# Kernel optimization log

Hardware: AMD Instinct MI355X
Metric: run time of the kernel (lower is better)

Reference implementation:

```python
import jax, jax.numpy as jnp
import numpy as np
from functools import partial

VOCAB = 32000
EMB = 512
HID = 1024
DEPTH = 2
B, S = 4, 512
PAD = 0


def _lstm_layer(x, mask, Wk, Wr, b):
    """Keras-style LSTM (gates i,f,g,o), return_sequences, zero init state.
    x: [B,S,D], mask: [B,S] bool. Masked steps carry state & output through."""
    Bdim = x.shape[0]
    units = Wr.shape[0]
    h0 = jnp.zeros((Bdim, units), x.dtype)
    c0 = jnp.zeros((Bdim, units), x.dtype)

    def step(carry, inp):
        h, c = carry
        xt, mt = inp                      # xt [B,D], mt [B]
        z = xt @ Wk + h @ Wr + b          # [B,4U]
        i, f, g, o = jnp.split(z, 4, axis=-1)
        i = jax.nn.sigmoid(i)
        f = jax.nn.sigmoid(f)
        g = jnp.tanh(g)
        o = jax.nn.sigmoid(o)
        c_new = f * c + i * g
        h_new = o * jnp.tanh(c_new)
        m = mt[:, None]
        h = jnp.where(m, h_new, h)
        c = jnp.where(m, c_new, c)
        return (h, c), h

    xs = jnp.swapaxes(x, 0, 1)            # [S,B,D]
    ms = jnp.swapaxes(mask, 0, 1)         # [S,B]
    _, ys = jax.lax.scan(step, (h0, c0), (xs, ms))
    return jnp.swapaxes(ys, 0, 1)         # [B,S,U]


def setup_inputs() -> dict:
    key = jax.random.key(0)
    ks = jax.random.split(key, 10)
    r = 0.02  # initializer_range
    inputs = jax.random.randint(ks[0], (B, S), 0, VOCAB, dtype=jnp.int32)
    emb = jax.random.normal(ks[1], (VOCAB, EMB), jnp.float32) * r
    Wk0 = jax.random.normal(ks[2], (EMB, 4 * HID), jnp.float32) * r
    Wr0 = jax.random.normal(ks[3], (HID, 4 * HID), jnp.float32) * r
    b0 = jnp.zeros((4 * HID,), jnp.float32)
    Wk1 = jax.random.normal(ks[4], (HID, 4 * HID), jnp.float32) * r
    Wr1 = jax.random.normal(ks[5], (HID, 4 * HID), jnp.float32) * r
    b1 = jnp.zeros((4 * HID,), jnp.float32)
    Wp = jax.random.normal(ks[6], (HID, EMB), jnp.float32) * r
    bp = jnp.zeros((EMB,), jnp.float32)
    return {"inputs": inputs, "emb": emb, "Wk0": Wk0, "Wr0": Wr0, "b0": b0,
            "Wk1": Wk1, "Wr1": Wr1, "b1": b1, "Wp": Wp, "bp": bp}


def reference(inputs, emb, Wk0, Wr0, b0, Wk1, Wr1, b1, Wp, bp):
    mask = inputs != PAD                          # [B,S] bool
    fmask = mask.astype(jnp.float32)[..., None]   # [B,S,1]
    x = emb[inputs]                               # [B,S,EMB] embedding lookup
    x = _lstm_layer(x, mask, Wk0, Wr0, b0)        # [B,S,HID]
    x = _lstm_layer(x, mask, Wk1, Wr1, b1)        # [B,S,HID]
    x = x @ Wp + bp                               # [B,S,EMB] output projection
    logits = jnp.einsum('bse,ve->bsv', x, emb)    # tied softmax weights
    onehot0 = jnp.zeros((VOCAB,), jnp.float32).at[0].set(1.0)  # eye(V)[0]
    logits = logits * fmask + onehot0 * (1.0 - fmask)
    return logits
```

## Files before the change

kernel.cpp:

```cpp
#include <hip/hip_runtime.h>

#define VOCAB 32000
#define EMBD  512
#define HIDD  1024
#define SLEN  512
#define NBAT  4
#define GATE4 4096
#define ABLK  128
#define BBLK  128

typedef unsigned long long u64;

#define AL(p) __hip_atomic_load((p), __ATOMIC_RELAXED, __HIP_MEMORY_SCOPE_AGENT)
#define AS(p, v) __hip_atomic_store((p), (v), __ATOMIC_RELAXED, __HIP_MEMORY_SCOPE_AGENT)

__device__ __forceinline__ float2 u2f(u64 x) {
  return make_float2(__uint_as_float((unsigned)x),
                     __uint_as_float((unsigned)(x >> 32)));
}

__global__ __launch_bounds__(256) void transpose_k(const float* __restrict__ src,
                                                   float* __restrict__ dst) {
  __shared__ float t[32][33];
  const int bx = blockIdx.x * 32;
  const int by = blockIdx.y * 32;
  const int r0 = threadIdx.x >> 5;
  const int c  = threadIdx.x & 31;
  #pragma unroll
  for (int i = 0; i < 4; i++) {
    const int r = r0 + i*8;
    t[r][c] = src[(size_t)(by + r)*GATE4 + bx + c];
  }
  __syncthreads();
  #pragma unroll
  for (int i = 0; i < 4; i++) {
    const int rw = r0 + i*8;
    dst[(size_t)(bx + rw)*HIDD + by + c] = t[c][rw];
  }
}

__global__ __launch_bounds__(256) void gemm_nn_emb(
    const int* __restrict__ ids, const float* __restrict__ emb,
    const float* __restrict__ B, const float* __restrict__ bias,
    float* __restrict__ C, int N, int K) {
  __shared__ float As[16][64];
  __shared__ float Bs[16][64];
  const int tid = threadIdx.x;
  const int bm = blockIdx.y * 64;
  const int bn = blockIdx.x * 64;
  const int tx = tid & 15, ty = tid >> 4;
  const int mA = tid >> 2, kqA = (tid & 3) * 4;
  const int kB = tid >> 4, nB = (tid & 15) * 4;
  const int rid = ids[bm + mA];
  float acc[4][4] = {{0.f}};
  for (int k0 = 0; k0 < K; k0 += 16) {
    float4 a4 = *(const float4*)(emb + (size_t)rid*EMBD + k0 + kqA);
    As[kqA+0][mA] = a4.x; As[kqA+1][mA] = a4.y;
    As[kqA+2][mA] = a4.z; As[kqA+3][mA] = a4.w;
    *(float4*)&Bs[kB][nB] = *(const float4*)(B + (size_t)(k0 + kB)*N + bn + nB);
    __syncthreads();
    #pragma unroll
    for (int k = 0; k < 16; k++) {
      float4 av = *(float4*)&As[k][ty*4];
      float4 bv = *(float4*)&Bs[k][tx*4];
      float ar[4] = {av.x, av.y, av.z, av.w};
      float br[4] = {bv.x, bv.y, bv.z, bv.w};
      #pragma unroll
      for (int i = 0; i < 4; i++)
        #pragma unroll
        for (int j = 0; j < 4; j++)
          acc[i][j] += ar[i] * br[j];
    }
    __syncthreads();
  }
  float4 bi = *(const float4*)(bias + bn + tx*4);
  #pragma unroll
  for (int i = 0; i < 4; i++) {
    float4 o;
    o.x = acc[i][0] + bi.x; o.y = acc[i][1] + bi.y;
    o.z = acc[i][2] + bi.z; o.w = acc[i][3] + bi.w;
    *(float4*)(C + (size_t)(bm + ty*4 + i)*N + bn + tx*4) = o;
  }
}

__global__ __launch_bounds__(256) void gemm_nn_bias(
    const float* __restrict__ A, const float* __restrict__ B,
    const float* __restrict__ bias, float* __restrict__ C,
    int M, int N, int K) {
  __shared__ float As[16][64];
  __shared__ float Bs[16][64];
  const int tid = threadIdx.x;
  const int bm = blockIdx.y * 64;
  const int bn = blockIdx.x * 64;
  const int tx = tid & 15, ty = tid >> 4;
  const int mA = tid >> 2, kqA = (tid & 3) * 4;
  const int kB = tid >> 4, nB = (tid & 15) * 4;
  float acc[4][4] = {{0.f}};
  for (int k0 = 0; k0 < K; k0 += 16) {
    float4 a4 = *(const float4*)(A + (size_t)(bm + mA)*K + k0 + kqA);
    As[kqA+0][mA] = a4.x; As[kqA+1][mA] = a4.y;
    As[kqA+2][mA] = a4.z; As[kqA+3][mA] = a4.w;
    *(float4*)&Bs[kB][nB] = *(const float4*)(B + (size_t)(k0 + kB)*N + bn + nB);
    __syncthreads();
    #pragma unroll
    for (int k = 0; k < 16; k++) {
      float4 av = *(float4*)&As[k][ty*4];
      float4 bv = *(float4*)&Bs[k][tx*4];
      float ar[4] = {av.x, av.y, av.z, av.w};
      float br[4] = {bv.x, bv.y, bv.z, bv.w};
      #pragma unroll
      for (int i = 0; i < 4; i++)
        #pragma unroll
        for (int j = 0; j < 4; j++)
          acc[i][j] += ar[i] * br[j];
    }
    __syncthreads();
  }
  float4 bi = *(const float4*)(bias + bn + tx*4);
  #pragma unroll
  for (int i = 0; i < 4; i++) {
    float4 o;
    o.x = acc[i][0] + bi.x; o.y = acc[i][1] + bi.y;
    o.z = acc[i][2] + bi.z; o.w = acc[i][3] + bi.w;
    *(float4*)(C + (size_t)(bm + ty*4 + i)*N + bn + tx*4) = o;
  }
}

__global__ __launch_bounds__(256) void gemm_nt_logits128(
    const float* __restrict__ A,
    const float* __restrict__ Bt,
    const int* __restrict__ ids,
    float* __restrict__ C) {
  const int K = EMBD, N = VOCAB;
  __shared__ float As[16][128];
  __shared__ float Bs[16][128];
  const int tid = threadIdx.x;
  const int bm = blockIdx.y * 128;
  const int bn = blockIdx.x * 128;
  const int tx = tid & 15, ty = tid >> 4;
  const int rL = tid >> 1, kL = (tid & 1) * 8;
  float acc[8][8] = {{0.f}};
  for (int k0 = 0; k0 < K; k0 += 16) {
    float4 a0 = *(const float4*)(A  + (size_t)(bm + rL)*K + k0 + kL);
    float4 a1 = *(const float4*)(A  + (size_t)(bm + rL)*K + k0 + kL + 4);
    float4 b0 = *(const float4*)(Bt + (size_t)(bn + rL)*K + k0 + kL);
    float4 b1 = *(const float4*)(Bt + (size_t)(bn + rL)*K + k0 + kL + 4);
    __syncthreads();
    As[kL+0][rL] = a0.x; As[kL+1][rL] = a0.y; As[kL+2][rL] = a0.z; As[kL+3][rL] = a0.w;
    As[kL+4][rL] = a1.x; As[kL+5][rL] = a1.y; As[kL+6][rL] = a1.z; As[kL+7][rL] = a1.w;
    Bs[kL+0][rL] = b0.x; Bs[kL+1][rL] = b0.y; Bs[kL+2][rL] = b0.z; Bs[kL+3][rL] = b0.w;
    Bs[kL+4][rL] = b1.x; Bs[kL+5][rL] = b1.y; Bs[kL+6][rL] = b1.z; Bs[kL+7][rL] = b1.w;
    __syncthreads();
    #pragma unroll
    for (int k = 0; k < 16; k++) {
      float4 av0 = *(float4*)&As[k][ty*4];
      float4 av1 = *(float4*)&As[k][64 + ty*4];
      float4 bv0 = *(float4*)&Bs[k][tx*4];
      float4 bv1 = *(float4*)&Bs[k][64 + tx*4];
      float ar[8] = {av0.x, av0.y, av0.z, av0.w, av1.x, av1.y, av1.z, av1.w};
      float br[8] = {bv0.x, bv0.y, bv0.z, bv0.w, bv1.x, bv1.y, bv1.z, bv1.w};
      #pragma unroll
      for (int i = 0; i < 8; i++)
        #pragma unroll
        for (int j = 0; j < 8; j++)
          acc[i][j] += ar[i] * br[j];
    }
  }
  #pragma unroll
  for (int i = 0; i < 8; i++) {
    const int row = bm + ((i < 4) ? (ty*4 + i) : (64 + ty*4 + i - 4));
    const bool mk = ids[row] != 0;
    float4 o0, o1;
    if (mk) {
      o0 = make_float4(acc[i][0], acc[i][1], acc[i][2], acc[i][3]);
      o1 = make_float4(acc[i][4], acc[i][5], acc[i][6], acc[i][7]);
    } else {
      o0 = make_float4((bn + tx*4 == 0) ? 1.f : 0.f, 0.f, 0.f, 0.f);
      o1 = make_float4(0.f, 0.f, 0.f, 0.f);
    }
    *(float4*)(C + (size_t)row*N + bn + tx*4)      = o0;
    *(float4*)(C + (size_t)row*N + bn + 64 + tx*4) = o1;
  }
}

__device__ __forceinline__ int rev5(int l) {
  return ((l & 1) << 4) | ((l & 2) << 2) | (l & 4) | ((l & 8) >> 2) | ((l & 16) >> 4);
}

#define HALVE(MASK, SH, HSZ)                          \
    { const int bit_ = (lane >> SH) & 1;              \
      _Pragma("unroll")                               \
      for (int j = 0; j < HSZ; j++) {                 \
        float snd = bit_ ? a[j] : a[j + HSZ];         \
        float kep = bit_ ? a[j + HSZ] : a[j];         \
        a[j] = kep + __shfl_xor(snd, MASK);           \
      } }

__global__ __launch_bounds__(256, 1) void lstm_fused(
    const float* __restrict__ Z0,
    const float* __restrict__ Wr0T,
    const float* __restrict__ Wk1T,
    const float* __restrict__ Wr1T,
    const float* __restrict__ bias1,
    const int* __restrict__ ids,
    float* __restrict__ H1,
    float* __restrict__ H0full,
    unsigned* __restrict__ flgA,
    unsigned* __restrict__ flgB) {
  __shared__ float wk[32][1024];
  __shared__ float z_s[4][64];
  __shared__ float zc[128];
  const int tid  = threadIdx.x;
  const int lane = tid & 63;
  const int w    = tid >> 6;
  const int ccH  = tid >> 7;
  const int part = tid & 127;

  if (blockIdx.x < ABLK) {
    const int hbase = blockIdx.x * 8;
    float4 Wf[16], Wg[16];
    #pragma unroll
    for (int cl = 0; cl < 16; cl++) {
      const int cc = ccH * 16 + cl;
      const int g  = cc >> 3, d = cc & 7;
      const size_t col = (size_t)(g * HIDD + hbase + d);
      Wf[cl] = *(const float4*)(Wr0T + col * HIDD + 4 * part);
      Wg[cl] = *(const float4*)(Wr0T + col * HIDD + 512 + 4 * part);
    }
    float c_reg = 0.f, h_reg = 0.f;
    __syncthreads();

    for (int t = 0; t < SLEN; t++) {
      float pz0 = 0.f, pz1 = 0.f, pz2 = 0.f, pz3 = 0.f;
      int pmk = 0;
      if (tid < 32) {
        const int b = tid >> 3, d = tid & 7;
        const float* zrow = Z0 + (size_t)(b*SLEN + t) * GATE4 + hbase + d;
        pz0 = zrow[0];      pz1 = zrow[HIDD];
        pz2 = zrow[2*HIDD]; pz3 = zrow[3*HIDD];
        pmk = ids[b*SLEN + t];
      }
      float4 ha[NBAT], hb[NBAT];
      if (t > 0) {
        if (tid < ABLK) {
          while (AL(flgA + tid * 16) < (unsigned)t)
            __builtin_amdgcn_s_sleep(1);
        }
        __syncthreads();
        const u64* src = (const u64*)H0full + (size_t)(t - 1) * 2048;
        u64 v[16];
        #pragma unroll
        for (int b = 0; b < NBAT; b++) {
          v[b*4+0] = AL(src + b*512 + 2*part);
          v[b*4+1] = AL(src + b*512 + 2*part + 1);
          v[b*4+2] = AL(src + b*512 + 256 + 2*part);
          v[b*4+3] = AL(src + b*512 + 256 + 2*part + 1);
        }
        #pragma unroll
        for (int b = 0; b < NBAT; b++) {
          float2 p0 = u2f(v[b*4+0]), p1 = u2f(v[b*4+1]);
          float2 q0 = u2f(v[b*4+2]), q1 = u2f(v[b*4+3]);
          ha[b] = make_float4(p0.x, p0.y, p1.x, p1.y);
          hb[b] = make_float4(q0.x, q0.y, q1.x, q1.y);
        }
      } else {
        #pragma unroll
        for (int b = 0; b < NBAT; b++) {
          ha[b] = make_float4(0.f, 0.f, 0.f, 0.f);
          hb[b] = make_float4(0.f, 0.f, 0.f, 0.f);
        }
      }
      float a[64];
      #pragma unroll
      for (int cl = 0; cl < 16; cl++)
        #pragma unroll
        for (int b = 0; b < NBAT; b++)
          a[cl*4 + b] = Wf[cl].x*ha[b].x + Wf[cl].y*ha[b].y
                      + Wf[cl].z*ha[b].z + Wf[cl].w*ha[b].w
                      + Wg[cl].x*hb[b].x + Wg[cl].y*hb[b].y
                      + Wg[cl].z*hb[b].z + Wg[cl].w*hb[b].w;
      #pragma unroll
      for (int i = 0; i < 64; i++) a[i] += __shfl_xor(a[i], 32);
      HALVE(1, 0, 32) HALVE(2, 1, 16) HALVE(4, 2, 8) HALVE(8, 3, 4) HALVE(16, 4, 2)
      if (lane < 32) {
        z_s[w][rev5(lane)*2 + 0] = a[0];
        z_s[w][rev5(lane)*2 + 1] = a[1];
      }
      __syncthreads();
      if (tid < 128) {
        const int cc = tid >> 2, b = tid & 3;
        const int cH = cc >> 4, i = ((cc & 15) << 2) | b;
        zc[tid] = z_s[2*cH][i] + z_s[2*cH + 1][i];
      }
      __syncthreads();
      if (tid < 32) {
        const int b = tid >> 3, d = tid & 7;
        const float zi = zc[((0*8 + d) << 2) + b] + pz0;
        const float zf = zc[((1*8 + d) << 2) + b] + pz1;
        const float zg = zc[((2*8 + d) << 2) + b] + pz2;
        const float zo = zc[((3*8 + d) << 2) + b] + pz3;
        const float ig = 1.f / (1.f + expf(-zi));
        const float fg = 1.f / (1.f + expf(-zf));
        const float gg = tanhf(zg);
        const float og = 1.f / (1.f + expf(-zo));
        const float cn = fg * c_reg + ig * gg;
        const float hn = og * tanhf(cn);
        const bool mk = pmk != 0;
        const float ho = mk ? hn : h_reg;
        c_reg = mk ? cn : c_reg;
        h_reg = ho;
        AS(H0full + (size_t)t * (NBAT*HIDD) + b*HIDD + hbase + d, ho);
      }
      if (w == 0) {
        asm volatile("s_waitcnt vmcnt(0)" ::: "memory");
        if (tid == 0)
          AS(flgA + blockIdx.x * 16, (unsigned)(t + 1));
      }
      __syncthreads();
    }
  } else {
    const int bid = blockIdx.x - ABLK;
    const int ub  = bid * 8;
    for (int i = tid; i < 32 * 256; i += 256) {
      const int c2 = i >> 8, k4 = i & 255;
      const size_t col = (size_t)((c2 >> 3) * HIDD + ub + (c2 & 7));
      *(float4*)&wk[c2][k4 * 4] = *(const float4*)(Wk1T + col * HIDD + 4 * k4);
    }
    float4 Rf[16], Rg[16];
    #pragma unroll
    for (int cl = 0; cl < 16; cl++) {
      const int cc = ccH * 16 + cl;
      const int g  = cc >> 3, d = cc & 7;
      const size_t col = (size_t)(g * HIDD + ub + d);
      Rf[cl] = *(const float4*)(Wr1T + col * HIDD + 4 * part);
      Rg[cl] = *(const float4*)(Wr1T + col * HIDD + 512 + 4 * part);
    }
    float pbi = 0.f, pbf = 0.f, pbg = 0.f, pbo = 0.f;
    if (tid < 32) {
      const int d = tid & 7;
      pbi = bias1[0*HIDD + ub + d];
      pbf = bias1[1*HIDD + ub + d];
      pbg = bias1[2*HIDD + ub + d];
      pbo = bias1[3*HIDD + ub + d];
    }
    float c_reg = 0.f, h_reg = 0.f;
    __syncthreads();

    for (int t = 0; t < SLEN; t++) {
      int pmk = 0;
      if (tid < 32) pmk = ids[(tid >> 3) * SLEN + t];
      if (tid < 128) {
        while (AL(flgA + tid * 16) < (unsigned)(t + 1))
          __builtin_amdgcn_s_sleep(1);
      } else {
        while (AL(flgB + (tid - 128) * 16) < (unsigned)t)
          __builtin_amdgcn_s_sleep(1);
      }
      __syncthreads();
      const u64* h0p = (const u64*)H0full + (size_t)t * 2048;
      u64 v0[16];
      #pragma unroll
      for (int b = 0; b < NBAT; b++) {
        v0[b*4+0] = AL(h0p + b*512 + 2*part);
        v0[b*4+1] = AL(h0p + b*512 + 2*part + 1);
        v0[b*4+2] = AL(h0p + b*512 + 256 + 2*part);
        v0[b*4+3] = AL(h0p + b*512 + 256 + 2*part + 1);
      }
      u64 v1[16];
      if (t > 0) {
        const u64* h1p = (const u64*)H1;
        #pragma unroll
        for (int b = 0; b < NBAT; b++) {
          const size_t row = (size_t)(b*SLEN + t - 1) * 512;
          v1[b*4+0] = AL(h1p + row + 2*part);
          v1[b*4+1] = AL(h1p + row + 2*part + 1);
          v1[b*4+2] = AL(h1p + row + 256 + 2*part);
          v1[b*4+3] = AL(h1p + row + 256 + 2*part + 1);
        }
      } else {
        #pragma unroll
        for (int r = 0; r < 16; r++) v1[r] = 0ull;
      }
      float a[64];
      #pragma unroll
      for (int cl = 0; cl < 16; cl++) {
        const int c2 = ccH * 16 + cl;
        const float4 kf = *(const float4*)&wk[c2][4 * part];
        const float4 kg = *(const float4*)&wk[c2][512 + 4 * part];
        #pragma unroll
        for (int b = 0; b < NBAT; b++) {
          const float2 p0 = u2f(v0[b*4+0]), p1 = u2f(v0[b*4+1]);
          const float2 q0 = u2f(v0[b*4+2]), q1 = u2f(v0[b*4+3]);
          a[cl*4 + b] = kf.x*p0.x + kf.y*p0.y + kf.z*p1.x + kf.w*p1.y
                      + kg.x*q0.x + kg.y*q0.y + kg.z*q1.x + kg.w*q1.y;
        }
      }
      #pragma unroll
      for (int cl = 0; cl < 16; cl++) {
        #pragma unroll
        for (int b = 0; b < NBAT; b++) {
          const float2 p0 = u2f(v1[b*4+0]), p1 = u2f(v1[b*4+1]);
          const float2 q0 = u2f(v1[b*4+2]), q1 = u2f(v1[b*4+3]);
          a[cl*4 + b] += Rf[cl].x*p0.x + Rf[cl].y*p0.y + Rf[cl].z*p1.x + Rf[cl].w*p1.y
                       + Rg[cl].x*q0.x + Rg[cl].y*q0.y + Rg[cl].z*q1.x + Rg[cl].w*q1.y;
        }
      }
      #pragma unroll
      for (int i = 0; i < 64; i++) a[i] += __shfl_xor(a[i], 32);
      HALVE(1, 0, 32) HALVE(2, 1, 16) HALVE(4, 2, 8) HALVE(8, 3, 4) HALVE(16, 4, 2)
      if (lane < 32) {
        z_s[w][rev5(lane)*2 + 0] = a[0];
        z_s[w][rev5(lane)*2 + 1] = a[1];
      }
      __syncthreads();
      if (tid < 128) {
        const int cc = tid >> 2, b = tid & 3;
        const int cH = cc >> 4, i = ((cc & 15) << 2) | b;
        zc[tid] = z_s[2*cH][i] + z_s[2*cH + 1][i];
      }
      __syncthreads();
      if (tid < 32) {
        const int b = tid >> 3, d = tid & 7;
        const float zi = zc[((0*8 + d) << 2) + b] + pbi;
        const float zf = zc[((1*8 + d) << 2) + b] + pbf;
        const float zg = zc[((2*8 + d) << 2) + b] + pbg;
        const float zo = zc[((3*8 + d) << 2) + b] + pbo;
        const float ig = 1.f / (1.f + expf(-zi));
        const float fg = 1.f / (1.f + expf(-zf));
        const float gg = tanhf(zg);
        const float og = 1.f / (1.f + expf(-zo));
        const float cn = fg * c_reg + ig * gg;
        const float hn = og * tanhf(cn);
        const bool mk = pmk != 0;
        const float ho = mk ? hn : h_reg;
        c_reg = mk ? cn : c_reg;
        h_reg = ho;
        AS(H1 + (size_t)(b*SLEN + t) * HIDD + ub + d, ho);
      }
      if (w == 0) {
        asm volatile("s_waitcnt vmcnt(0)" ::: "memory");
        if (tid == 0)
          AS(flgB + bid * 16, (unsigned)(t + 1));
      }
      __syncthreads();
    }
  }
}
#undef HALVE

extern "C" void kernel_launch(void* const* d_in, const int* in_sizes, int n_in,
                              void* d_out, int out_size, void* d_ws, size_t ws_size,
                              hipStream_t stream) {
  const int*   ids = (const int*)  d_in[0];
  const float* emb = (const float*)d_in[1];
  const float* Wk0 = (const float*)d_in[2];
  const float* Wr0 = (const float*)d_in[3];
  const float* b0  = (const float*)d_in[4];
  const float* Wk1 = (const float*)d_in[5];
  const float* Wr1 = (const float*)d_in[6];
  const float* b1  = (const float*)d_in[7];
  const float* Wp  = (const float*)d_in[8];
  const float* bp  = (const float*)d_in[9];
  float* out = (float*)d_out;

  float* Z      = out;
  float* H1     = out + 8388608;
  float* Wr0T   = out + 10485760;
  float* Wr1T   = out + 14680064;
  float* Wk1T   = out + 18874368;
  float* H0full = out + 23068672;
  unsigned* flgA = (unsigned*)d_ws;
  unsigned* flgB = (unsigned*)d_ws + 2048;
  float* P   = ((float*)d_ws) + 4096;

  hipMemsetAsync(d_ws, 0, 16384, stream);
  transpose_k<<<dim3(128, 32), 256, 0, stream>>>(Wr0, Wr0T);
  transpose_k<<<dim3(128, 32), 256, 0, stream>>>(Wr1, Wr1T);
  transpose_k<<<dim3(128, 32), 256, 0, stream>>>(Wk1, Wk1T);
  gemm_nn_emb<<<dim3(64, 32), 256, 0, stream>>>(ids, emb, Wk0, b0, Z, 4096, 512);
  lstm_fused<<<ABLK + BBLK, 256, 0, stream>>>(Z, Wr0T, Wk1T, Wr1T, b1, ids,
                                              H1, H0full, flgA, flgB);
  gemm_nn_bias<<<dim3(8, 32), 256, 0, stream>>>(H1, Wp, bp, P, 2048, 512, 1024);
  gemm_nt_logits128<<<dim3(250, 16), 256, 0, stream>>>(P, emb, ids, out);
}
```

Measured before the change: 4.819 ms.

## Stage hidden state through LDS with coalesced loads; split layer-1 wait for overlap

Hidden-state vectors (H0 and H1) are now loaded cooperatively by all 256 threads with contiguous 64-bit atomic loads, staged in a 16KB shared buffer, and read back as float4 per thread. Before, each thread issued strided per-batch atomic loads and many threads read the same data. In layer 1, the wait on layer-1 flags (flgB) is moved after the input-projection matmul on h0, so the h0 contribution is computed while the recurrent dependency resolves. The cost is extra __syncthreads barriers and more LDS use on top of a block that already holds 128KB of weights in LDS.

```diff
diff --git a/kernel.cpp b/kernel.cpp
--- a/kernel.cpp
+++ b/kernel.cpp
@@ -13,11 +13,6 @@
 
 #define AL(p) __hip_atomic_load((p), __ATOMIC_RELAXED, __HIP_MEMORY_SCOPE_AGENT)
 #define AS(p, v) __hip_atomic_store((p), (v), __ATOMIC_RELAXED, __HIP_MEMORY_SCOPE_AGENT)
-
-__device__ __forceinline__ float2 u2f(u64 x) {
-  return make_float2(__uint_as_float((unsigned)x),
-                     __uint_as_float((unsigned)(x >> 32)));
-}
 
 __global__ __launch_bounds__(256) void transpose_k(const float* __restrict__ src,
                                                    float* __restrict__ dst) {
@@ -208,6 +203,7 @@
     unsigned* __restrict__ flgA,
     unsigned* __restrict__ flgB) {
   __shared__ float wk[32][1024];
+  __shared__ float hs[NBAT * HIDD];
   __shared__ float z_s[4][64];
   __shared__ float zc[128];
   const int tid  = threadIdx.x;
@@ -248,20 +244,18 @@
         }
         __syncthreads();
         const u64* src = (const u64*)H0full + (size_t)(t - 1) * 2048;
-        u64 v[16];
+        u64 v[8];
+        #pragma unroll
+        for (int r = 0; r < 8; r++)
+          v[r] = AL(src + tid + (r << 8));
+        #pragma unroll
+        for (int r = 0; r < 8; r++)
+          ((u64*)hs)[tid + (r << 8)] = v[r];
+        __syncthreads();
         #pragma unroll
         for (int b = 0; b < NBAT; b++) {
-          v[b*4+0] = AL(src + b*512 + 2*part);
-          v[b*4+1] = AL(src + b*512 + 2*part + 1);
-          v[b*4+2] = AL(src + b*512 + 256 + 2*part);
-          v[b*4+3] = AL(src + b*512 + 256 + 2*part + 1);
-        }
-        #pragma unroll
-        for (int b = 0; b < NBAT; b++) {
-          float2 p0 = u2f(v[b*4+0]), p1 = u2f(v[b*4+1]);
-          float2 q0 = u2f(v[b*4+2]), q1 = u2f(v[b*4+3]);
-          ha[b] = make_float4(p0.x, p0.y, p1.x, p1.y);
-          hb[b] = make_float4(q0.x, q0.y, q1.x, q1.y);
+          ha[b] = *(const float4*)(hs + b*HIDD + 4*part);
+          hb[b] = *(const float4*)(hs + b*HIDD + 512 + 4*part);
         }
       } else {
         #pragma unroll
@@ -352,34 +346,24 @@
       if (tid < 128) {
         while (AL(flgA + tid * 16) < (unsigned)(t + 1))
           __builtin_amdgcn_s_sleep(1);
-      } else {
-        while (AL(flgB + (tid - 128) * 16) < (unsigned)t)
-          __builtin_amdgcn_s_sleep(1);
-      }
-      __syncthreads();
-      const u64* h0p = (const u64*)H0full + (size_t)t * 2048;
-      u64 v0[16];
+      }
+      __syncthreads();
+      {
+        const u64* h0p = (const u64*)H0full + (size_t)t * 2048;
+        u64 v[8];
+        #pragma unroll
+        for (int r = 0; r < 8; r++)
+          v[r] = AL(h0p + tid + (r << 8));
+        #pragma unroll
+        for (int r = 0; r < 8; r++)
+          ((u64*)hs)[tid + (r << 8)] = v[r];
+      }
+      __syncthreads();
+      float4 xa[NBAT], xb[NBAT];
       #pragma unroll
       for (int b = 0; b < NBAT; b++) {
-        v0[b*4+0] = AL(h0p + b*512 + 2*part);
-        v0[b*4+1] = AL(h0p + b*512 + 2*part + 1);
-        v0[b*4+2] = AL(h0p + b*512 + 256 + 2*part);
-        v0[b*4+3] = AL(h0p + b*512 + 256 + 2*part + 1);
-      }
-      u64 v1[16];
-      if (t > 0) {
-        const u64* h1p = (const u64*)H1;
-        #pragma unroll
-        for (int b = 0; b < NBAT; b++) {
-          const size_t row = (size_t)(b*SLEN + t - 1) * 512;
-          v1[b*4+0] = AL(h1p + row + 2*part);
-          v1[b*4+1] = AL(h1p + row + 2*part + 1);
-          v1[b*4+2] = AL(h1p + row + 256 + 2*part);
-          v1[b*4+3] = AL(h1p + row + 256 + 2*part + 1);
-        }
-      } else {
-        #pragma unroll
-        for (int r = 0; r < 16; r++) v1[r] = 0ull;
+        xa[b] = *(const float4*)(hs + b*HIDD + 4*part);
+        xb[b] = *(const float4*)(hs + b*HIDD + 512 + 4*part);
       }
       float a[64];
       #pragma unroll
@@ -389,20 +373,44 @@
         const float4 kg = *(const float4*)&wk[c2][512 + 4 * part];
         #pragma unroll
         for (int b = 0; b < NBAT; b++) {
-          const float2 p0 = u2f(v0[b*4+0]), p1 = u2f(v0[b*4+1]);
-          const float2 q0 = u2f(v0[b*4+2]), q1 = u2f(v0[b*4+3]);
-          a[cl*4 + b] = kf.x*p0.x + kf.y*p0.y + kf.z*p1.x + kf.w*p1.y
-                      + kg.x*q0.x + kg.y*q0.y + kg.z*q1.x + kg.w*q1.y;
-        }
-      }
-      #pragma unroll
-      for (int cl = 0; cl < 16; cl++) {
+          a[cl*4 + b] = kf.x*xa[b].x + kf.y*xa[b].y + kf.z*xa[b].z + kf.w*xa[b].w
+                      + kg.x*xb[b].x + kg.y*xb[b].y + kg.z*xb[b].z + kg.w*xb[b].w;
+        }
+      }
+      if (t > 0) {
+        if (tid < 128) {
+          while (AL(flgB + tid * 16) < (unsigned)t)
+            __builtin_amdgcn_s_sleep(1);
+        }
+        __syncthreads();
+        {
+          u64 v[8];
+          #pragma unroll
+          for (int r = 0; r < 8; r++) {
+            const int idx = tid + (r << 8);
+            const int b = idx >> 9, off = idx & 511;
+            v[r] = AL((const u64*)H1 + (size_t)(b*SLEN + t - 1) * 512 + off);
+          }
+          #pragma unroll
+          for (int r = 0; r < 8; r++)
+            ((u64*)hs)[tid + (r << 8)] = v[r];
+        }
+        __syncthreads();
+        float4 ya[NBAT], yb[NBAT];
         #pragma unroll
         for (int b = 0; b < NBAT; b++) {
-          const float2 p0 = u2f(v1[b*4+0]), p1 = u2f(v1[b*4+1]);
-          const float2 q0 = u2f(v1[b*4+2]), q1 = u2f(v1[b*4+3]);
-          a[cl*4 + b] += Rf[cl].x*p0.x + Rf[cl].y*p0.y + Rf[cl].z*p1.x + Rf[cl].w*p1.y
-                       + Rg[cl].x*q0.x + Rg[cl].y*q0.y + Rg[cl].z*q1.x + Rg[cl].w*q1.y;
+          ya[b] = *(const float4*)(hs + b*HIDD + 4*part);
+          yb[b] = *(const float4*)(hs + b*HIDD + 512 + 4*part);
+        }
+        #pragma unroll
+        for (int cl = 0; cl < 16; cl++) {
+          #pragma unroll
+          for (int b = 0; b < NBAT; b++) {
+            a[cl*4 + b] += Rf[cl].x*ya[b].x + Rf[cl].y*ya[b].y
+                         + Rf[cl].z*ya[b].z + Rf[cl].w*ya[b].w
+                         + Rg[cl].x*yb[b].x + Rg[cl].y*yb[b].y
+                         + Rg[cl].z*yb[b].z + Rg[cl].w*yb[b].w;
+          }
         }
       }
       #pragma unroll
```

New measurement: 4.204 ms. 1.15x faster.
